# Kernel optimization log

Measured on AMD Instinct MI355X. Metric: run time of the kernel, lower is better.

## Reference

```python
import jax, jax.numpy as jnp
import numpy as np

ALPHA = 0.2  # TF leaky_relu default

def setup_inputs() -> dict:
    key = jax.random.key(0)
    ks = jax.random.split(key, 6)
    B, N, F, D = 2, 8192, 256, 128
    seq = jax.random.normal(ks[0], (B, N, F), dtype=jnp.float32)
    # Conv1D with kernel size 1 == pointwise linear
    Wf = jax.random.normal(ks[1], (F, D), dtype=jnp.float32) * (1.0 / np.sqrt(F))
    w1 = jax.random.normal(ks[2], (D, 1), dtype=jnp.float32) * (1.0 / np.sqrt(D))
    b1 = jnp.zeros((1,), dtype=jnp.float32)
    w2 = jax.random.normal(ks[3], (D, 1), dtype=jnp.float32) * (1.0 / np.sqrt(D))
    b2 = jnp.zeros((1,), dtype=jnp.float32)
    bias = jnp.zeros((D,), dtype=jnp.float32)
    return {"seq": seq, "Wf": Wf, "w1": w1, "b1": b1, "w2": w2, "b2": b2, "bias": bias}

def reference(seq, Wf, w1, b1, w2, b2, bias):
    # seq: [B,N,F] -> seq_fts: [B,N,D]
    seq_fts = jnp.einsum('bnf,fd->bnd', seq, Wf)
    f1 = jnp.einsum('bnd,do->bno', seq_fts, w1) + b1  # [B,N,1]
    f2 = jnp.einsum('bnd,do->bno', seq_fts, w2) + b2  # [B,N,1]
    logits = f1 + jnp.swapaxes(f2, 1, 2)              # [B,N,N] outer-sum
    coefs = jax.nn.softmax(jax.nn.leaky_relu(logits, ALPHA), axis=-1)
    vals = jnp.einsum('bnm,bmd->bnd', coefs, seq_fts) + bias
    return jax.nn.leaky_relu(vals, ALPHA)
```

## Files before the change

### kernel.cpp

```cpp
#include <hip/hip_runtime.h>
#include <cstddef>

#define ALPHA 0.2f
constexpr int B = 2, N = 8192, F = 256, D = 128;
constexpr int M = B * N;
constexpr int NB = 2048;
constexpr int SUB = 128;
constexpr int P = N / SUB;
constexpr int GB = 2;
constexpr int NBB = NB / GB;
constexpr int GSZ = 64;
constexpr int NGRP = NB / GSZ;
constexpr int QROWS = 8;
constexpr int DSL = 4;
constexpr int NSL = D / DSL;
constexpr int BPT = NB / 128;

#define BMIN (-4.5f)
#define BSCALE ((float)NB / 9.0f)
__device__ inline int bucket_of(float x) {
  int g = (int)((x - BMIN) * BSCALE);
  return g < 0 ? 0 : (g > NB - 1 ? NB - 1 : g);
}

__global__ __launch_bounds__(512) void k_gemm(const float* __restrict__ seq,
                                              const float* __restrict__ Wf,
                                              const float* __restrict__ w1,
                                              const float* __restrict__ b1,
                                              const float* __restrict__ w2,
                                              const float* __restrict__ b2,
                                              float* __restrict__ fts,
                                              float* __restrict__ f1,
                                              float* __restrict__ f2) {
  __shared__ float As[32][68];
  __shared__ float Bs[32][128];
  const int m0 = blockIdx.x * 64;
  const int t = threadIdx.x;
  const int colg = t & 31;
  const int rowg = t >> 5;
  float acc[4][4];
#pragma unroll
  for (int r = 0; r < 4; ++r)
#pragma unroll
    for (int c = 0; c < 4; ++c) acc[r][c] = 0.f;

  for (int kc = 0; kc < F; kc += 32) {
    {
      const int row = t >> 3, k4 = t & 7;
      const float4 v = *reinterpret_cast<const float4*>(
          &seq[(size_t)(m0 + row) * F + kc + k4 * 4]);
      As[k4 * 4 + 0][row] = v.x; As[k4 * 4 + 1][row] = v.y;
      As[k4 * 4 + 2][row] = v.z; As[k4 * 4 + 3][row] = v.w;
    }
#pragma unroll
    for (int it = 0; it < 2; ++it) {
      const int f = t + it * 512;
      const int row = f >> 5, c4 = f & 31;
      *reinterpret_cast<float4*>(&Bs[row][c4 * 4]) =
          *reinterpret_cast<const float4*>(&Wf[(size_t)(kc + row) * D + c4 * 4]);
    }
    __syncthreads();
#pragma unroll
    for (int k = 0; k < 32; ++k) {
      const float4 a4 = *reinterpret_cast<const float4*>(&As[k][rowg * 4]);
      const float4 b4 = *reinterpret_cast<const float4*>(&Bs[k][colg * 4]);
      acc[0][0] += a4.x * b4.x; acc[0][1] += a4.x * b4.y; acc[0][2] += a4.x * b4.z; acc[0][3] += a4.x * b4.w;
      acc[1][0] += a4.y * b4.x; acc[1][1] += a4.y * b4.y; acc[1][2] += a4.y * b4.z; acc[1][3] += a4.y * b4.w;
      acc[2][0] += a4.z * b4.x; acc[2][1] += a4.z * b4.y; acc[2][2] += a4.z * b4.z; acc[2][3] += a4.z * b4.w;
      acc[3][0] += a4.w * b4.x; acc[3][1] += a4.w * b4.y; acc[3][2] += a4.w * b4.z; acc[3][3] += a4.w * b4.w;
    }
    __syncthreads();
  }
#pragma unroll
  for (int r = 0; r < 4; ++r) {
    float4 v = {acc[r][0], acc[r][1], acc[r][2], acc[r][3]};
    *reinterpret_cast<float4*>(&fts[(size_t)(m0 + rowg * 4 + r) * D + colg * 4]) = v;
  }
  const float w1v[4] = {w1[colg * 4], w1[colg * 4 + 1], w1[colg * 4 + 2], w1[colg * 4 + 3]};
  const float w2v[4] = {w2[colg * 4], w2[colg * 4 + 1], w2[colg * 4 + 2], w2[colg * 4 + 3]};
  const float b1v = b1[0], b2v = b2[0];
#pragma unroll
  for (int r = 0; r < 4; ++r) {
    float s1 = acc[r][0] * w1v[0] + acc[r][1] * w1v[1] + acc[r][2] * w1v[2] + acc[r][3] * w1v[3];
    float s2 = acc[r][0] * w2v[0] + acc[r][1] * w2v[1] + acc[r][2] * w2v[2] + acc[r][3] * w2v[3];
#pragma unroll
    for (int off = 16; off > 0; off >>= 1) {
      s1 += __shfl_down(s1, off, 32);
      s2 += __shfl_down(s2, off, 32);
    }
    if (colg == 0) {
      const int row = m0 + rowg * 4 + r;
      f1[row] = s1 + b1v;
      f2[row] = s2 + b2v;
    }
  }
}

__global__ __launch_bounds__(128) void k_hist(const float* __restrict__ f2,
                                              int* __restrict__ bid,
                                              int* __restrict__ histcnt) {
  __shared__ int hist[NB];
  const int b = blockIdx.x / P, p = blockIdx.x % P;
  const int t = threadIdx.x;
  for (int i = t; i < NB; i += 128) hist[i] = 0;
  const int j = p * SUB + t;
  float x = f2[b * N + j];
  int g = bucket_of(x);
  bid[b * N + j] = g;
  __syncthreads();
  atomicAdd(&hist[g], 1);
  __syncthreads();
  for (int i = t; i < NB; i += 128)
    histcnt[((size_t)(b * P + p)) * NB + i] = hist[i];
}

__global__ __launch_bounds__(256) void k_sub(const int* __restrict__ histcnt,
                                             int* __restrict__ substart,
                                             int* __restrict__ btot) {
  const int gid = blockIdx.x * 256 + threadIdx.x;
  const int b = gid / NB, g = gid % NB;
  int run = 0;
  for (int pp = 0; pp < P; ++pp) {
    substart[((size_t)(b * P + pp)) * NB + g] = run;
    run += histcnt[((size_t)(b * P + pp)) * NB + g];
  }
  btot[b * NB + g] = run;
}

__global__ __launch_bounds__(128) void k_scat(const float* __restrict__ f2,
                                              const int* __restrict__ bid,
                                              const int* __restrict__ substart,
                                              const int* __restrict__ btot,
                                              int* __restrict__ bstart,
                                              float4* __restrict__ kw,
                                              int* __restrict__ idxs) {
  __shared__ int bstart_lds[NB];
  __shared__ int bids[SUB];
  __shared__ int wsum2[2];
  const int b = blockIdx.x / P, p = blockIdx.x % P;
  const int t = threadIdx.x;
  const int lane = t & 63, wave = t >> 6;
  const size_t bN = (size_t)b * N;

  int c[BPT];
  int loc = 0;
#pragma unroll
  for (int i = 0; i < BPT; ++i) { c[i] = btot[b * NB + t * BPT + i]; loc += c[i]; }
  int incl = loc;
#pragma unroll
  for (int off = 1; off < 64; off <<= 1) {
    int y = __shfl_up(incl, off);
    if (lane >= off) incl += y;
  }
  if (lane == 63) wsum2[wave] = incl;
  __syncthreads();
  if (wave == 1) incl += wsum2[0];
  int excl = incl - loc;
#pragma unroll
  for (int i = 0; i < BPT; ++i) { bstart_lds[t * BPT + i] = excl; excl += c[i]; }
  __syncthreads();
  if (p == 0) {
    for (int i = t; i < NB; i += 128) bstart[b * (NB + 1) + i] = bstart_lds[i];
    if (t == 0) bstart[b * (NB + 1) + NB] = N;
  }

  const int j = p * SUB + t;
  const int g = bid[bN + j];
  bids[t] = g;
  __syncthreads();
  int off = bstart_lds[g] + substart[((size_t)(b * P + p)) * NB + g];
  for (int jj = 0; jj < t; ++jj) off += (bids[jj] == g);
  const float x = f2[bN + j];
  kw[bN + off] = make_float4(x, expf(x), expf(ALPHA * x), 0.f);
  idxs[bN + off] = j;
}

__global__ __launch_bounds__(256) void k_perm(const float* __restrict__ fts,
                                              const int* __restrict__ idxs,
                                              float* __restrict__ fts_s) {
  const int tid = blockIdx.x * 256 + threadIdx.x;
  const int eg = tid >> 5;
  const int q = tid & 31;
  const int b = eg / N;
  const int j = idxs[eg];
  *reinterpret_cast<float4*>(&fts_s[(size_t)eg * D + q * 4]) =
      *reinterpret_cast<const float4*>(&fts[((size_t)b * N + j) * D + q * 4]);
}

__global__ __launch_bounds__(128) void k_bsum(const float* __restrict__ fts_s,
                                              const float4* __restrict__ kw,
                                              const int* __restrict__ bstart,
                                              float* __restrict__ Wp, float* __restrict__ Wn,
                                              float* __restrict__ Cp, float* __restrict__ Cn) {
  const int b = blockIdx.x / NBB, blk = blockIdx.x % NBB;
  const int d = threadIdx.x;
  const int gbase = blk * GB;
  const size_t bN = (size_t)b * N;
  for (int gg = 0; gg < GB; ++gg) {
    const int g = gbase + gg;
    const int e0 = bstart[b * (NB + 1) + g], e1 = bstart[b * (NB + 1) + g + 1];
    float ap = 0.f, an = 0.f, sp = 0.f, sn = 0.f;
    int e = e0;
    for (; e + 4 <= e1; e += 4) {
      const float* vp = &fts_s[(bN + e) * D + d];
      const float v0 = vp[0], v1 = vp[D], v2 = vp[2 * D], v3 = vp[3 * D];
      const float4 k0 = kw[bN + e], k1 = kw[bN + e + 1], k2 = kw[bN + e + 2], k3 = kw[bN + e + 3];
      ap += k0.y * v0 + k1.y * v1 + k2.y * v2 + k3.y * v3;
      an += k0.z * v0 + k1.z * v1 + k2.z * v2 + k3.z * v3;
      sp += k0.y + k1.y + k2.y + k3.y;
      sn += k0.z + k1.z + k2.z + k3.z;
    }
    for (; e < e1; ++e) {
      const float v = fts_s[(bN + e) * D + d];
      const float4 k0 = kw[bN + e];
      ap += k0.y * v; an += k0.z * v; sp += k0.y; sn += k0.z;
    }
    Wp[((size_t)b * NB + g) * D + d] = ap;
    Wn[((size_t)b * NB + g) * D + d] = an;
    if (d == 0) { Cp[b * NB + g] = sp; Cn[b * NB + g] = sn; }
  }
}

__global__ __launch_bounds__(128) void k_scan(const float* __restrict__ Wp, const float* __restrict__ Wn,
                                              const float* __restrict__ Cp, const float* __restrict__ Cn,
                                              float* __restrict__ BPos, float* __restrict__ BNeg,
                                              float* __restrict__ CpB, float* __restrict__ CnB) {
  __shared__ float gp[NGRP][DSL], gn[NGRP][DSL];
  __shared__ float cgp[NGRP], cgn[NGRP];
  const int b = blockIdx.x / NSL, sl = blockIdx.x % NSL;
  const int t = threadIdx.x;
  const int d4 = t & (DSL - 1), grp = t >> 2;
  const int d = sl * DSL + d4;
  const size_t base = (size_t)b * NB;

  float sp = 0.f, sn = 0.f;
  for (int gg = 0; gg < GSZ; ++gg) {
    const int g = grp * GSZ + gg;
    sp += Wp[(base + g) * D + d];
    sn += Wn[(base + g) * D + d];
  }
  gp[grp][d4] = sp; gn[grp][d4] = sn;
  if (sl == 0 && d4 == 0) {
    float cp = 0.f, cn = 0.f;
    for (int gg = 0; gg < GSZ; ++gg) { const int g = grp * GSZ + gg; cp += Cp[base + g]; cn += Cn[base + g]; }
    cgp[grp] = cp; cgn[grp] = cn;
  }
  __syncthreads();

  if (t < DSL) {
    float run = 0.f;
    for (int g2 = 0; g2 < NGRP; ++g2) { const float v = gn[g2][t]; gn[g2][t] = run; run += v; }
  } else if (t < 2 * DSL) {
    const int dd = t - DSL;
    float run = 0.f;
    for (int g2 = NGRP - 1; g2 >= 0; --g2) { const float v = gp[g2][dd]; gp[g2][dd] = run; run += v; }
  } else if (sl == 0 && t == 2 * DSL) {
    float run = 0.f;
    for (int g2 = 0; g2 < NGRP; ++g2) { const float v = cgn[g2]; cgn[g2] = run; run += v; }
  } else if (sl == 0 && t == 2 * DSL + 1) {
    float run = 0.f;
    for (int g2 = NGRP - 1; g2 >= 0; --g2) { const float v = cgp[g2]; cgp[g2] = run; run += v; }
  }
  __syncthreads();

  float runn = gn[grp][d4];
  for (int gg = 0; gg < GSZ; ++gg) {
    const int g = grp * GSZ + gg;
    BNeg[(base + g) * D + d] = runn;
    runn += Wn[(base + g) * D + d];
  }
  float runp = gp[grp][d4];
  for (int gg = GSZ - 1; gg >= 0; --gg) {
    const int g = grp * GSZ + gg;
    BPos[(base + g) * D + d] = runp;
    runp += Wp[(base + g) * D + d];
  }
  if (sl == 0 && d4 == 0) {
    float rn = cgn[grp];
    for (int gg = 0; gg < GSZ; ++gg) { const int g = grp * GSZ + gg; CnB[base + g] = rn; rn += Cn[base + g]; }
    float rp = cgp[grp];
    for (int gg = GSZ - 1; gg >= 0; --gg) { const int g = grp * GSZ + gg; CpB[base + g] = rp; rp += Cp[base + g]; }
  }
}

__global__ __launch_bounds__(256) void k_query(const float* __restrict__ f1,
                                               const float4* __restrict__ kw,
                                               const float* __restrict__ fts_s,
                                               const int* __restrict__ bstart,
                                               const float* __restrict__ BPos, const float* __restrict__ BNeg,
                                               const float* __restrict__ CpB, const float* __restrict__ CnB,
                                               const float* __restrict__ bias,
                                               float* __restrict__ out) {
  const int r = threadIdx.x >> 5;
  const int lane = threadIdx.x & 31;
  const int row = blockIdx.x * QROWS + r;
  const int b = row / N;
  const size_t bN = (size_t)b * N;
  const int d4 = lane * 4;
  const float f1v = f1[row];
  const float th = -f1v;
  const int g = bucket_of(th);
  const int base = bstart[b * (NB + 1) + g];
  const int end  = bstart[b * (NB + 1) + g + 1];
  float4 sn = *reinterpret_cast<const float4*>(&BNeg[((size_t)b * NB + g) * D + d4]);
  float4 sp = *reinterpret_cast<const float4*>(&BPos[((size_t)b * NB + g) * D + d4]);
  float cn = CnB[b * NB + g];
  float cp = CpB[b * NB + g];
  for (int e = base; e < end; ++e) {
    const float4 kwe = kw[bN + e];
    const float4 v = *reinterpret_cast<const float4*>(&fts_s[(bN + e) * D + d4]);
    const bool neg = (kwe.x <= th);
    const float wn = neg ? kwe.z : 0.f;
    const float wp = neg ? 0.f : kwe.y;
    sn.x += wn * v.x; sn.y += wn * v.y; sn.z += wn * v.z; sn.w += wn * v.w;
    sp.x += wp * v.x; sp.y += wp * v.y; sp.z += wp * v.z; sp.w += wp * v.w;
    cn += wn; cp += wp;
  }
  const float wqp = expf(f1v), wqn = expf(ALPHA * f1v);
  const float denom = wqp * cp + wqn * cn;
  const float inv = 1.0f / denom;
  const float4 bi = *reinterpret_cast<const float4*>(&bias[d4]);
  float4 val;
  val.x = (wqp * sp.x + wqn * sn.x) * inv + bi.x;
  val.y = (wqp * sp.y + wqn * sn.y) * inv + bi.y;
  val.z = (wqp * sp.z + wqn * sn.z) * inv + bi.z;
  val.w = (wqp * sp.w + wqn * sn.w) * inv + bi.w;
  val.x = val.x >= 0.f ? val.x : ALPHA * val.x;
  val.y = val.y >= 0.f ? val.y : ALPHA * val.y;
  val.z = val.z >= 0.f ? val.z : ALPHA * val.z;
  val.w = val.w >= 0.f ? val.w : ALPHA * val.w;
  *reinterpret_cast<float4*>(&out[(size_t)row * D + d4]) = val;
}

extern "C" void kernel_launch(void* const* d_in, const int* in_sizes, int n_in,
                              void* d_out, int out_size, void* d_ws, size_t ws_size,
                              hipStream_t stream) {
  const float* seq  = (const float*)d_in[0];
  const float* Wf   = (const float*)d_in[1];
  const float* w1   = (const float*)d_in[2];
  const float* b1   = (const float*)d_in[3];
  const float* w2   = (const float*)d_in[4];
  const float* b2   = (const float*)d_in[5];
  const float* bias = (const float*)d_in[6];
  float* out = (float*)d_out;

  char* ws = (char*)d_ws;
  size_t off = 0;
  auto alloc = [&](size_t bytes) -> void* {
    void* p = ws + off;
    off = (off + bytes + 255) & ~(size_t)255;
    return p;
  };

  float*  fts     = (float*) alloc((size_t)M * D * 4);
  float*  fts_s   = (float*) alloc((size_t)M * D * 4);
  float*  f1      = (float*) alloc((size_t)M * 4);
  float*  f2      = (float*) alloc((size_t)M * 4);
  float4* kw      = (float4*)alloc((size_t)M * 16);
  int*    idxs    = (int*)   alloc((size_t)M * 4);
  int*    bid     = (int*)   alloc((size_t)M * 4);
  int*    histcnt = (int*)   alloc((size_t)B * P * NB * 4);
  int*    substart= (int*)   alloc((size_t)B * P * NB * 4);
  int*    btot    = (int*)   alloc((size_t)B * NB * 4);
  int*    bstart  = (int*)   alloc((size_t)B * (NB + 1) * 4);
  float*  Wp      = (float*) alloc((size_t)B * NB * D * 4);
  float*  Wn      = (float*) alloc((size_t)B * NB * D * 4);
  float*  Cp      = (float*) alloc((size_t)B * NB * 4);
  float*  Cn      = (float*) alloc((size_t)B * NB * 4);
  float*  BPos    = (float*) alloc((size_t)B * NB * D * 4);
  float*  BNeg    = (float*) alloc((size_t)B * NB * D * 4);
  float*  CpB     = (float*) alloc((size_t)B * NB * 4);
  float*  CnB     = (float*) alloc((size_t)B * NB * 4);

  hipLaunchKernelGGL(k_gemm,  dim3(M / 64),          dim3(512), 0, stream, seq, Wf, w1, b1, w2, b2, fts, f1, f2);
  hipLaunchKernelGGL(k_hist,  dim3(B * P),           dim3(128), 0, stream, f2, bid, histcnt);
  hipLaunchKernelGGL(k_sub,   dim3(B * NB / 256),    dim3(256), 0, stream, histcnt, substart, btot);
  hipLaunchKernelGGL(k_scat,  dim3(B * P),           dim3(128), 0, stream, f2, bid, substart, btot, bstart,
                     kw, idxs);
  hipLaunchKernelGGL(k_perm,  dim3(M * D / 4 / 256), dim3(256), 0, stream, fts, idxs, fts_s);
  hipLaunchKernelGGL(k_bsum,  dim3(B * NBB),         dim3(128), 0, stream, fts_s, kw, bstart, Wp, Wn, Cp, Cn);
  hipLaunchKernelGGL(k_scan,  dim3(B * NSL),         dim3(128), 0, stream, Wp, Wn, Cp, Cn, BPos, BNeg, CpB, CnB);
  hipLaunchKernelGGL(k_query, dim3(M / QROWS),       dim3(256), 0, stream, f1, kw, fts_s, bstart,
                     BPos, BNeg, CpB, CnB, bias, out);
}
```

Before: 86.32 us.

## Split bucket prefix scan into parallel chunk-sum and chunk-final kernels; shrink histogram counts

Result: slower. 103.9 us (+20.4%).

```diff
diff --git a/kernel.cpp b/kernel.cpp
--- a/kernel.cpp
+++ b/kernel.cpp
@@ -9,12 +9,10 @@
 constexpr int P = N / SUB;
 constexpr int GB = 2;
 constexpr int NBB = NB / GB;
-constexpr int GSZ = 64;
-constexpr int NGRP = NB / GSZ;
 constexpr int QROWS = 8;
-constexpr int DSL = 4;
-constexpr int NSL = D / DSL;
 constexpr int BPT = NB / 128;
+constexpr int CH = 16;
+constexpr int NCH = NB / CH;
 
 #define BMIN (-4.5f)
 #define BSCALE ((float)NB / 9.0f)
@@ -98,7 +96,7 @@
 
 __global__ __launch_bounds__(128) void k_hist(const float* __restrict__ f2,
                                               int* __restrict__ bid,
-                                              int* __restrict__ histcnt) {
+                                              unsigned short* __restrict__ histcnt) {
   __shared__ int hist[NB];
   const int b = blockIdx.x / P, p = blockIdx.x % P;
   const int t = threadIdx.x;
@@ -111,17 +109,17 @@
   atomicAdd(&hist[g], 1);
   __syncthreads();
   for (int i = t; i < NB; i += 128)
-    histcnt[((size_t)(b * P + p)) * NB + i] = hist[i];
-}
-
-__global__ __launch_bounds__(256) void k_sub(const int* __restrict__ histcnt,
-                                             int* __restrict__ substart,
+    histcnt[((size_t)(b * P + p)) * NB + i] = (unsigned short)hist[i];
+}
+
+__global__ __launch_bounds__(256) void k_sub(const unsigned short* __restrict__ histcnt,
+                                             unsigned short* __restrict__ substart,
                                              int* __restrict__ btot) {
   const int gid = blockIdx.x * 256 + threadIdx.x;
   const int b = gid / NB, g = gid % NB;
   int run = 0;
   for (int pp = 0; pp < P; ++pp) {
-    substart[((size_t)(b * P + pp)) * NB + g] = run;
+    substart[((size_t)(b * P + pp)) * NB + g] = (unsigned short)run;
     run += histcnt[((size_t)(b * P + pp)) * NB + g];
   }
   btot[b * NB + g] = run;
@@ -129,7 +127,7 @@
 
 __global__ __launch_bounds__(128) void k_scat(const float* __restrict__ f2,
                                               const int* __restrict__ bid,
-                                              const int* __restrict__ substart,
+                                              const unsigned short* __restrict__ substart,
                                               const int* __restrict__ btot,
                                               int* __restrict__ bstart,
                                               float4* __restrict__ kw,
@@ -168,7 +166,7 @@
   const int g = bid[bN + j];
   bids[t] = g;
   __syncthreads();
-  int off = bstart_lds[g] + substart[((size_t)(b * P + p)) * NB + g];
+  int off = bstart_lds[g] + (int)substart[((size_t)(b * P + p)) * NB + g];
   for (int jj = 0; jj < t; ++jj) off += (bids[jj] == g);
   const float x = f2[bN + j];
   kw[bN + off] = make_float4(x, expf(x), expf(ALPHA * x), 0.f);
@@ -221,65 +219,61 @@
   }
 }
 
-__global__ __launch_bounds__(128) void k_scan(const float* __restrict__ Wp, const float* __restrict__ Wn,
-                                              const float* __restrict__ Cp, const float* __restrict__ Cn,
-                                              float* __restrict__ BPos, float* __restrict__ BNeg,
-                                              float* __restrict__ CpB, float* __restrict__ CnB) {
-  __shared__ float gp[NGRP][DSL], gn[NGRP][DSL];
-  __shared__ float cgp[NGRP], cgn[NGRP];
-  const int b = blockIdx.x / NSL, sl = blockIdx.x % NSL;
-  const int t = threadIdx.x;
-  const int d4 = t & (DSL - 1), grp = t >> 2;
-  const int d = sl * DSL + d4;
+__global__ __launch_bounds__(128) void k_chsum(const float* __restrict__ Wp, const float* __restrict__ Wn,
+                                               const float* __restrict__ Cp, const float* __restrict__ Cn,
+                                               float* __restrict__ CSp, float* __restrict__ CSn,
+                                               float* __restrict__ CCp, float* __restrict__ CCn) {
+  const int b = blockIdx.x / NCH, ch = blockIdx.x % NCH;
+  const int d = threadIdx.x;
   const size_t base = (size_t)b * NB;
-
   float sp = 0.f, sn = 0.f;
-  for (int gg = 0; gg < GSZ; ++gg) {
-    const int g = grp * GSZ + gg;
+  for (int gg = 0; gg < CH; ++gg) {
+    const int g = ch * CH + gg;
     sp += Wp[(base + g) * D + d];
     sn += Wn[(base + g) * D + d];
   }
-  gp[grp][d4] = sp; gn[grp][d4] = sn;
-  if (sl == 0 && d4 == 0) {
+  CSp[((size_t)b * NCH + ch) * D + d] = sp;
+  CSn[((size_t)b * NCH + ch) * D + d] = sn;
+  if (d == 0) {
     float cp = 0.f, cn = 0.f;
-    for (int gg = 0; gg < GSZ; ++gg) { const int g = grp * GSZ + gg; cp += Cp[base + g]; cn += Cn[base + g]; }
-    cgp[grp] = cp; cgn[grp] = cn;
-  }
-  __syncthreads();
-
-  if (t < DSL) {
-    float run = 0.f;
-    for (int g2 = 0; g2 < NGRP; ++g2) { const float v = gn[g2][t]; gn[g2][t] = run; run += v; }
-  } else if (t < 2 * DSL) {
-    const int dd = t - DSL;
-    float run = 0.f;
-    for (int g2 = NGRP - 1; g2 >= 0; --g2) { const float v = gp[g2][dd]; gp[g2][dd] = run; run += v; }
-  } else if (sl == 0 && t == 2 * DSL) {
-    float run = 0.f;
-    for (int g2 = 0; g2 < NGRP; ++g2) { const float v = cgn[g2]; cgn[g2] = run; run += v; }
-  } else if (sl == 0 && t == 2 * DSL + 1) {
-    float run = 0.f;
-    for (int g2 = NGRP - 1; g2 >= 0; --g2) { const float v = cgp[g2]; cgp[g2] = run; run += v; }
-  }
-  __syncthreads();
-
-  float runn = gn[grp][d4];
-  for (int gg = 0; gg < GSZ; ++gg) {
-    const int g = grp * GSZ + gg;
+    for (int gg = 0; gg < CH; ++gg) { const int g = ch * CH + gg; cp += Cp[base + g]; cn += Cn[base + g]; }
+    CCp[b * NCH + ch] = cp; CCn[b * NCH + ch] = cn;
+  }
+}
+
+__global__ __launch_bounds__(128) void k_chfinal(const float* __restrict__ Wp, const float* __restrict__ Wn,
+                                                 const float* __restrict__ Cp, const float* __restrict__ Cn,
+                                                 const float* __restrict__ CSp, const float* __restrict__ CSn,
+                                                 const float* __restrict__ CCp, const float* __restrict__ CCn,
+                                                 float* __restrict__ BPos, float* __restrict__ BNeg,
+                                                 float* __restrict__ CpB, float* __restrict__ CnB) {
+  const int b = blockIdx.x / NCH, ch = blockIdx.x % NCH;
+  const int d = threadIdx.x;
+  const size_t base = (size_t)b * NB;
+  const size_t cbase = (size_t)b * NCH;
+  float offn = 0.f, offp = 0.f;
+  for (int c2 = 0; c2 < ch; ++c2)        offn += CSn[(cbase + c2) * D + d];
+  for (int c2 = ch + 1; c2 < NCH; ++c2)  offp += CSp[(cbase + c2) * D + d];
+  float runn = offn;
+  for (int gg = 0; gg < CH; ++gg) {
+    const int g = ch * CH + gg;
     BNeg[(base + g) * D + d] = runn;
     runn += Wn[(base + g) * D + d];
   }
-  float runp = gp[grp][d4];
-  for (int gg = GSZ - 1; gg >= 0; --gg) {
-    const int g = grp * GSZ + gg;
+  float runp = offp;
+  for (int gg = CH - 1; gg >= 0; --gg) {
+    const int g = ch * CH + gg;
     BPos[(base + g) * D + d] = runp;
     runp += Wp[(base + g) * D + d];
   }
-  if (sl == 0 && d4 == 0) {
-    float rn = cgn[grp];
-    for (int gg = 0; gg < GSZ; ++gg) { const int g = grp * GSZ + gg; CnB[base + g] = rn; rn += Cn[base + g]; }
-    float rp = cgp[grp];
-    for (int gg = GSZ - 1; gg >= 0; --gg) { const int g = grp * GSZ + gg; CpB[base + g] = rp; rp += Cp[base + g]; }
+  if (d == 0) {
+    float on = 0.f, op = 0.f;
+    for (int c2 = 0; c2 < ch; ++c2)       on += CCn[cbase + c2];
+    for (int c2 = ch + 1; c2 < NCH; ++c2) op += CCp[cbase + c2];
+    float rn = on;
+    for (int gg = 0; gg < CH; ++gg) { const int g = ch * CH + gg; CnB[base + g] = rn; rn += Cn[base + g]; }
+    float rp = op;
+    for (int gg = CH - 1; gg >= 0; --gg) { const int g = ch * CH + gg; CpB[base + g] = rp; rp += Cp[base + g]; }
   }
 }
 
@@ -359,27 +353,33 @@
   float4* kw      = (float4*)alloc((size_t)M * 16);
   int*    idxs    = (int*)   alloc((size_t)M * 4);
   int*    bid     = (int*)   alloc((size_t)M * 4);
-  int*    histcnt = (int*)   alloc((size_t)B * P * NB * 4);
-  int*    substart= (int*)   alloc((size_t)B * P * NB * 4);
+  unsigned short* histcnt  = (unsigned short*)alloc((size_t)B * P * NB * 2);
+  unsigned short* substart = (unsigned short*)alloc((size_t)B * P * NB * 2);
   int*    btot    = (int*)   alloc((size_t)B * NB * 4);
   int*    bstart  = (int*)   alloc((size_t)B * (NB + 1) * 4);
   float*  Wp      = (float*) alloc((size_t)B * NB * D * 4);
   float*  Wn      = (float*) alloc((size_t)B * NB * D * 4);
   float*  Cp      = (float*) alloc((size_t)B * NB * 4);
   float*  Cn      = (float*) alloc((size_t)B * NB * 4);
+  float*  CSp     = (float*) alloc((size_t)B * NCH * D * 4);
+  float*  CSn     = (float*) alloc((size_t)B * NCH * D * 4);
+  float*  CCp     = (float*) alloc((size_t)B * NCH * 4);
+  float*  CCn     = (float*) alloc((size_t)B * NCH * 4);
   float*  BPos    = (float*) alloc((size_t)B * NB * D * 4);
   float*  BNeg    = (float*) alloc((size_t)B * NB * D * 4);
   float*  CpB     = (float*) alloc((size_t)B * NB * 4);
   float*  CnB     = (float*) alloc((size_t)B * NB * 4);
 
-  hipLaunchKernelGGL(k_gemm,  dim3(M / 64),          dim3(512), 0, stream, seq, Wf, w1, b1, w2, b2, fts, f1, f2);
-  hipLaunchKernelGGL(k_hist,  dim3(B * P),           dim3(128), 0, stream, f2, bid, histcnt);
-  hipLaunchKernelGGL(k_sub,   dim3(B * NB / 256),    dim3(256), 0, stream, histcnt, substart, btot);
-  hipLaunchKernelGGL(k_scat,  dim3(B * P),           dim3(128), 0, stream, f2, bid, substart, btot, bstart,
+  hipLaunchKernelGGL(k_gemm,    dim3(M / 64),          dim3(512), 0, stream, seq, Wf, w1, b1, w2, b2, fts, f1, f2);
+  hipLaunchKernelGGL(k_hist,    dim3(B * P),           dim3(128), 0, stream, f2, bid, histcnt);
+  hipLaunchKernelGGL(k_sub,     dim3(B * NB / 256),    dim3(256), 0, stream, histcnt, substart, btot);
+  hipLaunchKernelGGL(k_scat,    dim3(B * P),           dim3(128), 0, stream, f2, bid, substart, btot, bstart,
                      kw, idxs);
-  hipLaunchKernelGGL(k_perm,  dim3(M * D / 4 / 256), dim3(256), 0, stream, fts, idxs, fts_s);
-  hipLaunchKernelGGL(k_bsum,  dim3(B * NBB),         dim3(128), 0, stream, fts_s, kw, bstart, Wp, Wn, Cp, Cn);
-  hipLaunchKernelGGL(k_scan,  dim3(B * NSL),         dim3(128), 0, stream, Wp, Wn, Cp, Cn, BPos, BNeg, CpB, CnB);
-  hipLaunchKernelGGL(k_query, dim3(M / QROWS),       dim3(256), 0, stream, f1, kw, fts_s, bstart,
+  hipLaunchKernelGGL(k_perm,    dim3(M * D / 4 / 256), dim3(256), 0, stream, fts, idxs, fts_s);
+  hipLaunchKernelGGL(k_bsum,    dim3(B * NBB),         dim3(128), 0, stream, fts_s, kw, bstart, Wp, Wn, Cp, Cn);
+  hipLaunchKernelGGL(k_chsum,   dim3(B * NCH),         dim3(128), 0, stream, Wp, Wn, Cp, Cn, CSp, CSn, CCp, CCn);
+  hipLaunchKernelGGL(k_chfinal, dim3(B * NCH),         dim3(128), 0, stream, Wp, Wn, Cp, Cn, CSp, CSn, CCp, CCn,
+                     BPos, BNeg, CpB, CnB);
+  hipLaunchKernelGGL(k_query,   dim3(M / QROWS),       dim3(256), 0, stream, f1, kw, fts_s, bstart,
                      BPos, BNeg, CpB, CnB, bias, out);
 }
```
